# Performance work log

Hardware: AMD Instinct MI355X
Metric: run time of the kernel (lower is better)

Reference implementation:

```python
import jax, jax.numpy as jnp
import numpy as np

N_HEAD = 16
ROPE_BASE = 10000.0
RMS_EPS = 1e-6

def rms_norm(x):
    # F.rms_norm(x, (x.size(-1),)) -- no learned weight
    return x * jax.lax.rsqrt(jnp.mean(x * x, axis=-1, keepdims=True) + RMS_EPS)

def rope(x):
    # x: [B, T, H, hd]; rotate halves (non-interleaved) like the torch Rotary
    T, hd = x.shape[1], x.shape[3]
    d = hd // 2
    inv_freq = 1.0 / (ROPE_BASE ** (jnp.arange(0, hd, 2, dtype=jnp.float32) / hd))  # [d]
    t = jnp.arange(T, dtype=jnp.float32)
    freqs = jnp.outer(t, inv_freq)                       # [T, d]
    cos = jnp.cos(freqs)[None, :, None, :]
    sin = jnp.sin(freqs)[None, :, None, :]
    x1, x2 = x[..., :d], x[..., d:]
    y1 = x1 * cos + x2 * sin
    y2 = -x1 * sin + x2 * cos
    return jnp.concatenate([y1, y2], axis=-1).astype(x.dtype)

def setup_inputs() -> dict:
    key = jax.random.key(0)
    ks = jax.random.split(key, 7)
    B, T, D, H = 2, 2048, 1024, N_HEAD
    hd = D // H
    s = 0.02
    return {
        "x": jax.random.normal(ks[0], (B, T, D), jnp.float32),
        "v1": jax.random.normal(ks[1], (B, T, H, hd), jnp.float32),
        "w_q": jax.random.normal(ks[2], (D, D), jnp.float32) * s,
        "w_k": jax.random.normal(ks[3], (D, D), jnp.float32) * s,
        "w_v": jax.random.normal(ks[4], (D, D), jnp.float32) * s,
        "w_proj": jax.random.normal(ks[5], (D, D), jnp.float32) * s,
        "lamb": jnp.float32(0.5),
    }

def reference(x, v1, w_q, w_k, w_v, w_proj, lamb):
    B, T, D = x.shape
    H = N_HEAD
    hd = D // H
    q = (x @ w_q.T).reshape(B, T, H, hd)
    k = (x @ w_k.T).reshape(B, T, H, hd)
    v = (x @ w_v.T).reshape(B, T, H, hd)
    v = (1.0 - lamb) * v + lamb * v1.reshape(B, T, H, hd)
    q, k = rms_norm(q), rms_norm(k)
    q, k = rope(q), rope(k)
    scale = 1.0 / jnp.sqrt(jnp.float32(hd))
    scores = jnp.einsum('bqhd,bkhd->bhqk', q, k) * scale  # [B,H,T,T]
    causal = jnp.tril(jnp.ones((T, T), dtype=bool))
    scores = jnp.where(causal[None, None], scores, jnp.float32(-1e30))
    attn = jax.nn.softmax(scores, axis=-1)
    y = jnp.einsum('bhqk,bkhd->bqhd', attn, v).reshape(B, T, D)
    y = y @ w_proj.T
    return (y, v1)
```

## Files before the change

### kernel.cpp

```cpp
#include <hip/hip_runtime.h>

typedef __bf16 bf16x8 __attribute__((ext_vector_type(8)));
typedef float f32x4 __attribute__((ext_vector_type(4)));
typedef float f32x16 __attribute__((ext_vector_type(16)));

__device__ __forceinline__ unsigned short f2bf(float f) {
    return __builtin_bit_cast(unsigned short, (__bf16)f);
}

__device__ __forceinline__ float bf2f(unsigned short u) {
    unsigned int x = ((unsigned int)u) << 16;
    return __builtin_bit_cast(float, x);
}

__device__ __forceinline__ unsigned int packbf2(float a, float b) {
    unsigned short lo = f2bf(a), hi = f2bf(b);
    return (unsigned int)lo | ((unsigned int)hi << 16);
}

__device__ __forceinline__ bf16x8 load_frag(const unsigned short* p) {
    int4 v = *reinterpret_cast<const int4*>(p);
    return __builtin_bit_cast(bf16x8, v);
}

__device__ __forceinline__ void gload_lds16(const unsigned short* g, unsigned short* l) {
    __builtin_amdgcn_global_load_lds((const __attribute__((address_space(1))) void*)g,
                                     (__attribute__((address_space(3))) void*)l, 16, 0, 0);
}

__global__ __launch_bounds__(256) void prep_bf16(const float* __restrict__ x,
                                                 const float* __restrict__ wq,
                                                 const float* __restrict__ wk,
                                                 const float* __restrict__ wv,
                                                 const float* __restrict__ wp,
                                                 unsigned short* __restrict__ xb,
                                                 unsigned short* __restrict__ wall,
                                                 float* __restrict__ cost,
                                                 float* __restrict__ sint) {
    int bid = blockIdx.x;
    if (bid < 8192) {
        int i = (bid * 256 + threadIdx.x) * 4;
        const float* src;
        unsigned short* dst;
        int soff, doff;
        if (i < (1 << 22)) {
            src = x; dst = xb; soff = i; doff = i;
        } else {
            int j = i - (1 << 22);
            int r = j >> 20;
            src = (r == 0) ? wq : ((r == 1) ? wk : ((r == 2) ? wv : wp));
            dst = wall; soff = j & 1048575; doff = j;
        }
        float4 v = *reinterpret_cast<const float4*>(&src[soff]);
        unsigned short tmp[4] = {f2bf(v.x), f2bf(v.y), f2bf(v.z), f2bf(v.w)};
        *reinterpret_cast<int2*>(&dst[doff]) = *reinterpret_cast<int2*>(tmp);
    } else {
        int i = (bid - 8192) * 256 + threadIdx.x;
        int t = i >> 5, d = i & 31;
        float inv = powf(10000.0f, -(float)d / 32.0f);
        float f = (float)t * inv;
        cost[i] = cosf(f);
        sint[i] = sinf(f);
    }
}

template <bool BF16OUT>
__global__ __launch_bounds__(256) void gemm_bf16(const unsigned short* __restrict__ A,
                                                 const unsigned short* __restrict__ B,
                                                 void* __restrict__ Cv,
                                                 int N, int K) {
    __shared__ __align__(16) unsigned short As[128 * 64];
    __shared__ __align__(16) unsigned short Bs[128 * 64];
    int tid = threadIdx.x;
    int lane = tid & 63;
    int w = tid >> 6;
    int wm = w >> 1, wn = w & 1;
    int m0 = blockIdx.x * 128;
    int n0 = blockIdx.y * 128;

    f32x4 acc[4][4] = {};

    int r8 = lane >> 3;
    int csrc = (lane & 7) ^ r8;

    for (int k0 = 0; k0 < K; k0 += 64) {
        __syncthreads();
#pragma unroll
        for (int c = 0; c < 4; ++c) {
            int row = 32 * w + 8 * c + r8;
            gload_lds16(&A[(size_t)(m0 + row) * K + k0 + csrc * 8], &As[(32 * w + 8 * c) * 64]);
            gload_lds16(&B[(size_t)(n0 + row) * K + k0 + csrc * 8], &Bs[(32 * w + 8 * c) * 64]);
        }
        __syncthreads();
#pragma unroll
        for (int kk = 0; kk < 2; ++kk) {
            int col16 = kk * 4 + (lane >> 4);
            bf16x8 af[4], bfr[4];
#pragma unroll
            for (int i = 0; i < 4; ++i) {
                int row = wm * 64 + i * 16 + (lane & 15);
                af[i] = load_frag(&As[row * 64 + (col16 ^ (row & 7)) * 8]);
            }
#pragma unroll
            for (int j = 0; j < 4; ++j) {
                int row = wn * 64 + j * 16 + (lane & 15);
                bfr[j] = load_frag(&Bs[row * 64 + (col16 ^ (row & 7)) * 8]);
            }
#pragma unroll
            for (int i = 0; i < 4; ++i)
#pragma unroll
                for (int j = 0; j < 4; ++j)
                    acc[i][j] = __builtin_amdgcn_mfma_f32_16x16x32_bf16(af[i], bfr[j], acc[i][j], 0, 0, 0);
        }
    }
    int r0 = (lane >> 4) * 4;
    int cc = lane & 15;
#pragma unroll
    for (int i = 0; i < 4; ++i)
#pragma unroll
        for (int j = 0; j < 4; ++j)
#pragma unroll
            for (int r = 0; r < 4; ++r) {
                size_t m = m0 + wm * 64 + i * 16 + r0 + r;
                size_t n = n0 + wn * 64 + j * 16 + cc;
                if constexpr (BF16OUT) {
                    ((unsigned short*)Cv)[m * N + n] = f2bf(acc[i][j][r]);
                } else {
                    ((float*)Cv)[m * N + n] = acc[i][j][r];
                }
            }
}

__global__ __launch_bounds__(256) void post_lerp(const unsigned short* __restrict__ qkv,
                                                 const float* __restrict__ cost,
                                                 const float* __restrict__ sint,
                                                 const float* __restrict__ v1,
                                                 const float* __restrict__ lamb_p,
                                                 unsigned short* __restrict__ qb,
                                                 unsigned short* __restrict__ kb,
                                                 unsigned short* __restrict__ vt,
                                                 float* __restrict__ outv1) {
    __shared__ __align__(16) unsigned short tile[64][72];
    int bid = blockIdx.x;
    if (bid < 16384) {
        int gid = bid * 4 + (threadIdx.x >> 6);
        int lane = threadIdx.x & 63;
        int h = gid & 15;
        int t = (gid >> 4) & 2047;
        int b = gid >> 15;
        int m = b * 2048 + t;

        float q = bf2f(qkv[(size_t)m * 3072 + h * 64 + lane]);
        float k = bf2f(qkv[(size_t)m * 3072 + 1024 + h * 64 + lane]);

        float sq = q * q, sk = k * k;
        for (int msk = 1; msk < 64; msk <<= 1) {
            sq += __shfl_xor(sq, msk, 64);
            sk += __shfl_xor(sk, msk, 64);
        }
        q *= rsqrtf(sq * (1.0f / 64.0f) + 1e-6f);
        k *= rsqrtf(sk * (1.0f / 64.0f) + 1e-6f);

        int d = lane & 31;
        float c = cost[t * 32 + d], s = sint[t * 32 + d];
        float qp = __shfl_xor(q, 32, 64);
        float kp = __shfl_xor(k, 32, 64);
        float qo = (lane < 32) ? (q * c + qp * s) : (q * c - qp * s);
        float ko = (lane < 32) ? (k * c + kp * s) : (k * c - kp * s);
        qo *= 0.125f * 1.44269504088896f;

        size_t oidx = ((size_t)((b * 16 + h) * 2048 + t)) * 64 + lane;
        qb[oidx] = f2bf(qo);
        kb[oidx] = f2bf(ko);
    } else {
        int b2 = bid - 16384;
        int bh = b2 >> 5;
        int b = bh >> 4, h = bh & 15;
        int t0 = (b2 & 31) * 64;
        int tid = threadIdx.x;
        int r = tid >> 3;
        int c = (tid & 7) * 8;
        float lamb = lamb_p[0];
        float oml = 1.0f - lamb;

#pragma unroll
        for (int half = 0; half < 2; ++half) {
            int row = r + half * 32;
            int m = b * 2048 + t0 + row;
            int4 vv = *reinterpret_cast<const int4*>(&qkv[(size_t)m * 3072 + 2048 + h * 64 + c]);
            const unsigned short* vs = reinterpret_cast<const unsigned short*>(&vv);
            size_t v1i = ((size_t)m * 16 + h) * 64 + c;
            float4 va = *reinterpret_cast<const float4*>(&v1[v1i]);
            float4 vb4 = *reinterpret_cast<const float4*>(&v1[v1i + 4]);
            *reinterpret_cast<float4*>(&outv1[v1i]) = va;
            *reinterpret_cast<float4*>(&outv1[v1i + 4]) = vb4;
            float v1a[8] = {va.x, va.y, va.z, va.w, vb4.x, vb4.y, vb4.z, vb4.w};
            unsigned short tmp[8];
#pragma unroll
            for (int j = 0; j < 8; ++j) tmp[j] = f2bf(oml * bf2f(vs[j]) + lamb * v1a[j]);
            *reinterpret_cast<int4*>(&tile[row][c]) = *reinterpret_cast<int4*>(tmp);
        }
        __syncthreads();
        unsigned short* dst = vt + (size_t)bh * 64 * 2048 + t0;
        unsigned short tmp[8];
#pragma unroll
        for (int j = 0; j < 8; ++j) tmp[j] = tile[c + j][r];
        *reinterpret_cast<int4*>(&dst[(size_t)r * 2048 + c]) = *reinterpret_cast<int4*>(tmp);
#pragma unroll
        for (int j = 0; j < 8; ++j) tmp[j] = tile[c + j][r + 32];
        *reinterpret_cast<int4*>(&dst[(size_t)(r + 32) * 2048 + c]) = *reinterpret_cast<int4*>(tmp);
    }
}

__global__ __launch_bounds__(256) void attn(const unsigned short* __restrict__ qb,
                                            const unsigned short* __restrict__ kb,
                                            const unsigned short* __restrict__ vt,
                                            unsigned short* __restrict__ pO,
                                            float* __restrict__ lsum) {
    __shared__ __align__(16) unsigned short Ks[64][72];
    __shared__ __align__(16) unsigned short Vt[64][72];
    int tid = threadIdx.x;
    int lane = tid & 63;
    int w = tid >> 6;
    int hi = lane >> 5;
    int l31 = lane & 31;

    int bid = blockIdx.x;
    int bh = bid & 31;
    int r6 = bid >> 5;
    int qt = 15 - (r6 >> 2);
    int ck = r6 & 3;
    int q0 = qt * 128;
    const size_t base = (size_t)bh * 2048 * 64;
    const unsigned short* vtb = vt + (size_t)bh * 64 * 2048;
    int nt = 2 * qt + 2;
    int ktlo = (ck * nt) >> 2;
    int kthi = ((ck + 1) * nt) >> 2;

    bf16x8 qf[4];
    int qrow = q0 + w * 32 + l31;
#pragma unroll
    for (int kd = 0; kd < 4; ++kd)
        qf[kd] = load_frag(&qb[base + (size_t)qrow * 64 + kd * 16 + hi * 8]);

    f32x16 oacc[2] = {};
    float lrun = 0.0f;

    int srow = tid >> 3;
    int scol = (tid & 7) * 8;
    int4 kr0, kr1, vr0, vr1;
#define LOADT(kt_)                                                                                    \
    do {                                                                                              \
        kr0 = *reinterpret_cast<const int4*>(&kb[base + (size_t)((kt_)*64 + srow) * 64 + scol]);      \
        kr1 = *reinterpret_cast<const int4*>(&kb[base + (size_t)((kt_)*64 + srow + 32) * 64 + scol]); \
        vr0 = *reinterpret_cast<const int4*>(&vtb[(size_t)srow * 2048 + (kt_)*64 + scol]);            \
        vr1 = *reinterpret_cast<const int4*>(&vtb[(size_t)(srow + 32) * 2048 + (kt_)*64 + scol]);     \
    } while (0)

    int qwlo = q0 + w * 32;
    if (ktlo < kthi) {
        LOADT(ktlo);
        for (int kt = ktlo; kt < kthi; ++kt) {
            __syncthreads();
            *reinterpret_cast<int4*>(&Ks[srow][scol]) = kr0;
            *reinterpret_cast<int4*>(&Ks[srow + 32][scol]) = kr1;
            *reinterpret_cast<int4*>(&Vt[srow][scol]) = vr0;
            *reinterpret_cast<int4*>(&Vt[srow + 32][scol]) = vr1;
            __syncthreads();
            if (kt + 1 < kthi) LOADT(kt + 1);

            if (kt * 64 <= qwlo + 31) {
                bool diag = (kt * 64 + 63 > qwlo);
                float rs01 = 0.0f, rs23 = 0.0f;
#pragma unroll
                for (int ntl = 0; ntl < 2; ++ntl) {
                    f32x16 sacc = {};
#pragma unroll
                    for (int kd = 0; kd < 4; ++kd) {
                        bf16x8 kf = load_frag(&Ks[ntl * 32 + l31][kd * 16 + hi * 8]);
                        sacc = __builtin_amdgcn_mfma_f32_32x32x16_bf16(kf, qf[kd], sacc, 0, 0, 0);
                    }

#pragma unroll
                    for (int r = 0; r < 16; ++r) {
                        float s = sacc[r];
                        if (diag) {
                            int kvg = kt * 64 + ntl * 32 + (r & 3) + 8 * (r >> 2) + 4 * hi;
                            if (kvg > qrow) s = -3.0e38f;
                        }
                        float e = __builtin_amdgcn_exp2f(s);
                        sacc[r] = e;
                        if (r & 2) rs23 += e; else rs01 += e;
                    }

                    unsigned int wAa[4], wBb[4];
#pragma unroll
                    for (int rr = 0; rr < 4; ++rr) {
                        wAa[rr] = packbf2(sacc[4 * rr + 0], sacc[4 * rr + 1]);
                        wBb[rr] = packbf2(sacc[4 * rr + 2], sacc[4 * rr + 3]);
                    }

#pragma unroll
                    for (int ks2 = 0; ks2 < 2; ++ks2) {
                        int b2 = ks2 * 2;
                        auto rA = __builtin_amdgcn_permlane32_swap(wAa[b2], wAa[b2 + 1], false, false);
                        auto rB = __builtin_amdgcn_permlane32_swap(wBb[b2], wBb[b2 + 1], false, false);
                        uint4 pa;
                        pa.x = rA[0];
                        pa.y = rB[0];
                        pa.z = rA[1];
                        pa.w = rB[1];
                        bf16x8 paf = __builtin_bit_cast(bf16x8, pa);
                        int ks = ntl * 2 + ks2;
#pragma unroll
                        for (int dt = 0; dt < 2; ++dt) {
                            bf16x8 vtf = load_frag(&Vt[dt * 32 + l31][ks * 16 + hi * 8]);
                            oacc[dt] = __builtin_amdgcn_mfma_f32_32x32x16_bf16(paf, vtf, oacc[dt], 0, 0, 0);
                        }
                    }
                }
                float rs = rs01 + rs23;
                rs += __shfl_xor(rs, 32, 64);
                lrun += rs;
            }
        }
    }

    unsigned short* po = pO + ((size_t)ck * 4194304u);
    float* ls = lsum + ck * 65536;
#pragma unroll
    for (int r = 0; r < 16; ++r) {
        int ql = (r & 3) + 8 * (r >> 2) + 4 * hi;
        int q = q0 + w * 32 + ql;
        size_t ro = ((size_t)bh * 2048 + q) * 64;
        po[ro + l31]      = f2bf(oacc[0][r]);
        po[ro + 32 + l31] = f2bf(oacc[1][r]);
    }
    if (hi == 0) ls[bh * 2048 + q0 + w * 32 + l31] = lrun;
#undef LOADT
}

__global__ __launch_bounds__(256) void combine(const unsigned short* __restrict__ pO,
                                               const float* __restrict__ lsum,
                                               unsigned short* __restrict__ yb) {
    int g = blockIdx.x * 256 + threadIdx.x;
    int d8 = (g & 7) * 8;
    int q  = (g >> 3) & 2047;
    int bh = g >> 14;
    int b = bh >> 4, h = bh & 15;
    size_t pi = ((size_t)bh * 2048 + q) * 64 + d8;
    int4 p0 = *reinterpret_cast<const int4*>(&pO[pi]);
    int4 p1 = *reinterpret_cast<const int4*>(&pO[4194304u + pi]);
    int4 p2 = *reinterpret_cast<const int4*>(&pO[8388608u + pi]);
    int4 p3 = *reinterpret_cast<const int4*>(&pO[12582912u + pi]);
    int li = bh * 2048 + q;
    float l = lsum[li] + lsum[65536 + li] + lsum[131072 + li] + lsum[196608 + li];
    float linv = 1.0f / l;
    const unsigned short* u0 = reinterpret_cast<const unsigned short*>(&p0);
    const unsigned short* u1 = reinterpret_cast<const unsigned short*>(&p1);
    const unsigned short* u2 = reinterpret_cast<const unsigned short*>(&p2);
    const unsigned short* u3 = reinterpret_cast<const unsigned short*>(&p3);
    unsigned short tmp[8];
#pragma unroll
    for (int j = 0; j < 8; ++j)
        tmp[j] = f2bf(((bf2f(u0[j]) + bf2f(u1[j])) + (bf2f(u2[j]) + bf2f(u3[j]))) * linv);
    *reinterpret_cast<int4*>(&yb[((size_t)(b * 2048 + q) * 16 + h) * 64 + d8]) =
        *reinterpret_cast<int4*>(tmp);
}

extern "C" void kernel_launch(void* const* d_in, const int* in_sizes, int n_in,
                              void* d_out, int out_size, void* d_ws, size_t ws_size,
                              hipStream_t stream) {
    const float* x      = (const float*)d_in[0];
    const float* v1     = (const float*)d_in[1];
    const float* w_q    = (const float*)d_in[2];
    const float* w_k    = (const float*)d_in[3];
    const float* w_v    = (const float*)d_in[4];
    const float* w_proj = (const float*)d_in[5];
    const float* lamb   = (const float*)d_in[6];
    float* out = (float*)d_out;

    char* ws = (char*)d_ws;
    unsigned short* xb      = (unsigned short*)(ws + 0);
    unsigned short* wall_b  = (unsigned short*)(ws + (8u  << 20));
    unsigned short* wqkv_b  = wall_b;
    unsigned short* wproj_b = wall_b + 3u * 1048576u;
    unsigned short* qkvb    = (unsigned short*)(ws + (16u << 20));
    unsigned short* vtp     = (unsigned short*)(ws + (40u << 20));
    unsigned short* qbuf    = (unsigned short*)(ws + (48u << 20));
    unsigned short* kbuf    = (unsigned short*)(ws + (56u << 20));
    unsigned short* ybuf    = (unsigned short*)(ws + (64u << 20));
    float*          cost    = (float*)        (ws + (72u << 20));
    float*          sint    = (float*)        (ws + (72u << 20) + 262144);
    unsigned short* pO      = (unsigned short*)(ws + (80u << 20));
    float*          lsum    = (float*)        (ws + (112u << 20));

    prep_bf16<<<8448, 256, 0, stream>>>(x, w_q, w_k, w_v, w_proj, xb, wall_b, cost, sint);

    gemm_bf16<true><<<dim3(32, 24), 256, 0, stream>>>(xb, wqkv_b, (void*)qkvb, 3072, 1024);

    post_lerp<<<17408, 256, 0, stream>>>(qkvb, cost, sint, v1, lamb, qbuf, kbuf, vtp, out + 4194304);

    attn<<<2048, 256, 0, stream>>>(qbuf, kbuf, vtp, pO, lsum);
    combine<<<2048, 256, 0, stream>>>(pO, lsum, ybuf);

    gemm_bf16<false><<<dim3(32, 8), 256, 0, stream>>>(ybuf, wproj_b, (void*)out, 1024, 1024);
}
```

Before: 134.0 us.

## Fuse split-K combine into projection GEMM and halve attention key splits

Attention now splits each query tile's key range into 2 chunks instead of 4, which halves the attn grid and the partial-output buffers. The separate combine kernel is removed. The output-projection GEMM now loads the two bf16 partial outputs and row sums, normalizes them, and writes the A tile straight into shared memory. This drops one launch and the ybuf write/read round trip. In exchange there is less attention parallelism per query tile, and the A-tile load in the GEMM does more work without async copy.

```diff
diff --git a/kernel.cpp b/kernel.cpp
--- a/kernel.cpp
+++ b/kernel.cpp
@@ -64,10 +64,9 @@
     }
 }
 
-template <bool BF16OUT>
 __global__ __launch_bounds__(256) void gemm_bf16(const unsigned short* __restrict__ A,
                                                  const unsigned short* __restrict__ B,
-                                                 void* __restrict__ Cv,
+                                                 unsigned short* __restrict__ C,
                                                  int N, int K) {
     __shared__ __align__(16) unsigned short As[128 * 64];
     __shared__ __align__(16) unsigned short Bs[128 * 64];
@@ -123,11 +122,84 @@
             for (int r = 0; r < 4; ++r) {
                 size_t m = m0 + wm * 64 + i * 16 + r0 + r;
                 size_t n = n0 + wn * 64 + j * 16 + cc;
-                if constexpr (BF16OUT) {
-                    ((unsigned short*)Cv)[m * N + n] = f2bf(acc[i][j][r]);
-                } else {
-                    ((float*)Cv)[m * N + n] = acc[i][j][r];
-                }
+                C[m * N + n] = f2bf(acc[i][j][r]);
+            }
+}
+
+__global__ __launch_bounds__(256) void gemm_proj(const unsigned short* __restrict__ pO,
+                                                 const float* __restrict__ lsum,
+                                                 const unsigned short* __restrict__ B,
+                                                 float* __restrict__ C) {
+    __shared__ __align__(16) unsigned short As[128 * 64];
+    __shared__ __align__(16) unsigned short Bs[128 * 64];
+    int tid = threadIdx.x;
+    int lane = tid & 63;
+    int w = tid >> 6;
+    int wm = w >> 1, wn = w & 1;
+    int m0 = blockIdx.x * 128;
+    int n0 = blockIdx.y * 128;
+
+    f32x4 acc[4][4] = {};
+
+    int r8 = lane >> 3;
+    int c8 = lane & 7;
+    int csrc = c8 ^ r8;
+
+    for (int k0 = 0; k0 < 1024; k0 += 64) {
+        int h = k0 >> 6;
+        __syncthreads();
+#pragma unroll
+        for (int c = 0; c < 4; ++c) {
+            int row = 32 * w + 8 * c + r8;
+            int m = m0 + row;
+            int bh = ((m >> 11) << 4) + h;
+            int qi = m & 2047;
+            int li = bh * 2048 + qi;
+            size_t pi = (size_t)li * 64 + csrc * 8;
+            int4 p0 = *reinterpret_cast<const int4*>(&pO[pi]);
+            int4 p1 = *reinterpret_cast<const int4*>(&pO[4194304u + pi]);
+            float linv = 1.0f / (lsum[li] + lsum[65536 + li]);
+            const unsigned short* u0 = reinterpret_cast<const unsigned short*>(&p0);
+            const unsigned short* u1 = reinterpret_cast<const unsigned short*>(&p1);
+            unsigned short tmp[8];
+#pragma unroll
+            for (int j = 0; j < 8; ++j) tmp[j] = f2bf((bf2f(u0[j]) + bf2f(u1[j])) * linv);
+            *reinterpret_cast<int4*>(&As[row * 64 + c8 * 8]) = *reinterpret_cast<int4*>(tmp);
+            gload_lds16(&B[(size_t)(n0 + row) * 1024 + k0 + csrc * 8], &Bs[(32 * w + 8 * c) * 64]);
+        }
+        __syncthreads();
+#pragma unroll
+        for (int kk = 0; kk < 2; ++kk) {
+            int col16 = kk * 4 + (lane >> 4);
+            bf16x8 af[4], bfr[4];
+#pragma unroll
+            for (int i = 0; i < 4; ++i) {
+                int row = wm * 64 + i * 16 + (lane & 15);
+                af[i] = load_frag(&As[row * 64 + (col16 ^ (row & 7)) * 8]);
+            }
+#pragma unroll
+            for (int j = 0; j < 4; ++j) {
+                int row = wn * 64 + j * 16 + (lane & 15);
+                bfr[j] = load_frag(&Bs[row * 64 + (col16 ^ (row & 7)) * 8]);
+            }
+#pragma unroll
+            for (int i = 0; i < 4; ++i)
+#pragma unroll
+                for (int j = 0; j < 4; ++j)
+                    acc[i][j] = __builtin_amdgcn_mfma_f32_16x16x32_bf16(af[i], bfr[j], acc[i][j], 0, 0, 0);
+        }
+    }
+    int r0 = (lane >> 4) * 4;
+    int cc = lane & 15;
+#pragma unroll
+    for (int i = 0; i < 4; ++i)
+#pragma unroll
+        for (int j = 0; j < 4; ++j)
+#pragma unroll
+            for (int r = 0; r < 4; ++r) {
+                size_t m = m0 + wm * 64 + i * 16 + r0 + r;
+                size_t n = n0 + wn * 64 + j * 16 + cc;
+                C[m * 1024 + n] = acc[i][j][r];
             }
 }
 
@@ -227,15 +299,14 @@
 
     int bid = blockIdx.x;
     int bh = bid & 31;
-    int r6 = bid >> 5;
-    int qt = 15 - (r6 >> 2);
-    int ck = r6 & 3;
+    int r5 = bid >> 5;
+    int qt = 15 - (r5 >> 1);
+    int ck = r5 & 1;
     int q0 = qt * 128;
     const size_t base = (size_t)bh * 2048 * 64;
     const unsigned short* vtb = vt + (size_t)bh * 64 * 2048;
-    int nt = 2 * qt + 2;
-    int ktlo = (ck * nt) >> 2;
-    int kthi = ((ck + 1) * nt) >> 2;
+    int ktlo = ck * (qt + 1);
+    int kthi = (ck + 1) * (qt + 1);
 
     bf16x8 qf[4];
     int qrow = q0 + w * 32 + l31;
@@ -258,7 +329,7 @@
     } while (0)
 
     int qwlo = q0 + w * 32;
-    if (ktlo < kthi) {
+    {
         LOADT(ktlo);
         for (int kt = ktlo; kt < kthi; ++kt) {
             __syncthreads();
@@ -340,34 +411,6 @@
 #undef LOADT
 }
 
-__global__ __launch_bounds__(256) void combine(const unsigned short* __restrict__ pO,
-                                               const float* __restrict__ lsum,
-                                               unsigned short* __restrict__ yb) {
-    int g = blockIdx.x * 256 + threadIdx.x;
-    int d8 = (g & 7) * 8;
-    int q  = (g >> 3) & 2047;
-    int bh = g >> 14;
-    int b = bh >> 4, h = bh & 15;
-    size_t pi = ((size_t)bh * 2048 + q) * 64 + d8;
-    int4 p0 = *reinterpret_cast<const int4*>(&pO[pi]);
-    int4 p1 = *reinterpret_cast<const int4*>(&pO[4194304u + pi]);
-    int4 p2 = *reinterpret_cast<const int4*>(&pO[8388608u + pi]);
-    int4 p3 = *reinterpret_cast<const int4*>(&pO[12582912u + pi]);
-    int li = bh * 2048 + q;
-    float l = lsum[li] + lsum[65536 + li] + lsum[131072 + li] + lsum[196608 + li];
-    float linv = 1.0f / l;
-    const unsigned short* u0 = reinterpret_cast<const unsigned short*>(&p0);
-    const unsigned short* u1 = reinterpret_cast<const unsigned short*>(&p1);
-    const unsigned short* u2 = reinterpret_cast<const unsigned short*>(&p2);
-    const unsigned short* u3 = reinterpret_cast<const unsigned short*>(&p3);
-    unsigned short tmp[8];
-#pragma unroll
-    for (int j = 0; j < 8; ++j)
-        tmp[j] = f2bf(((bf2f(u0[j]) + bf2f(u1[j])) + (bf2f(u2[j]) + bf2f(u3[j]))) * linv);
-    *reinterpret_cast<int4*>(&yb[((size_t)(b * 2048 + q) * 16 + h) * 64 + d8]) =
-        *reinterpret_cast<int4*>(tmp);
-}
-
 extern "C" void kernel_launch(void* const* d_in, const int* in_sizes, int n_in,
                               void* d_out, int out_size, void* d_ws, size_t ws_size,
                               hipStream_t stream) {
@@ -389,7 +432,6 @@
     unsigned short* vtp     = (unsigned short*)(ws + (40u << 20));
     unsigned short* qbuf    = (unsigned short*)(ws + (48u << 20));
     unsigned short* kbuf    = (unsigned short*)(ws + (56u << 20));
-    unsigned short* ybuf    = (unsigned short*)(ws + (64u << 20));
     float*          cost    = (float*)        (ws + (72u << 20));
     float*          sint    = (float*)        (ws + (72u << 20) + 262144);
     unsigned short* pO      = (unsigned short*)(ws + (80u << 20));
@@ -397,12 +439,11 @@
 
     prep_bf16<<<8448, 256, 0, stream>>>(x, w_q, w_k, w_v, w_proj, xb, wall_b, cost, sint);
 
-    gemm_bf16<true><<<dim3(32, 24), 256, 0, stream>>>(xb, wqkv_b, (void*)qkvb, 3072, 1024);
+    gemm_bf16<<<dim3(32, 24), 256, 0, stream>>>(xb, wqkv_b, qkvb, 3072, 1024);
 
     post_lerp<<<17408, 256, 0, stream>>>(qkvb, cost, sint, v1, lamb, qbuf, kbuf, vtp, out + 4194304);
 
-    attn<<<2048, 256, 0, stream>>>(qbuf, kbuf, vtp, pO, lsum);
-    combine<<<2048, 256, 0, stream>>>(pO, lsum, ybuf);
-
-    gemm_bf16<false><<<dim3(32, 8), 256, 0, stream>>>(ybuf, wproj_b, (void*)out, 1024, 1024);
-}
+    attn<<<1024, 256, 0, stream>>>(qbuf, kbuf, vtp, pO, lsum);
+
+    gemm_proj<<<dim3(32, 8), 256, 0, stream>>>(pO, lsum, wproj_b, out);
+}
```

Result: no change. 134.1 us (+0.0%).
